# Kernel optimization log

Measured on AMD Instinct MI355X. Metric: run time of the kernel, lower is better.

## Reference

```python
import jax, jax.numpy as jnp
import numpy as np

NUM_LAYERS = 3

def setup_inputs() -> dict:
    key = jax.random.key(0)
    ku, ki, ke1, ke2 = jax.random.split(key, 4)
    num_users, num_items, D, E = 100000, 50000, 128, 1000000
    # xavier-uniform-ish init scale for the embedding tables
    bound = float(np.sqrt(6.0 / (num_users + D)))
    user_w = jax.random.uniform(ku, (num_users, D), jnp.float32, -bound, bound)
    bound_i = float(np.sqrt(6.0 / (num_items + D)))
    item_w = jax.random.uniform(ki, (num_items, D), jnp.float32, -bound_i, bound_i)
    # bipartite edges: user -> item (item ids offset by num_users), plus reverse direction
    u = jax.random.randint(ke1, (E,), 0, num_users, dtype=jnp.int32)
    v = jax.random.randint(ke2, (E,), 0, num_items, dtype=jnp.int32) + num_users
    edge_index = jnp.stack([jnp.concatenate([u, v]), jnp.concatenate([v, u])])  # [2, 2E]
    return {"user_w": user_w, "item_w": item_w, "edge_index": edge_index,
            "num_users": num_users, "num_items": num_items}

def reference(user_w, item_w, edge_index, num_users, num_items):
    n_nodes = num_users + num_items
    src, dst = edge_index[0], edge_index[1]
    # degree via scatter-add (duplicate edges sum, same as coalesce)
    deg = jax.ops.segment_sum(jnp.ones_like(src, dtype=user_w.dtype), src,
                              num_segments=n_nodes)
    dinv = jnp.where(deg > 0, deg ** -0.5, 0.0)
    dinv = jnp.where(jnp.isfinite(dinv), dinv, 0.0)
    vals = dinv[src] * dinv[dst]  # normalized adjacency values, [2E]

    emb = jnp.concatenate([user_w, item_w], axis=0)  # [n_nodes, D]
    acc = emb
    x = emb
    for _ in range(NUM_LAYERS):
        # SpMM: out[s] += vals(e) * x[dst(e)]
        x = jax.ops.segment_sum(vals[:, None] * x[dst], src, num_segments=n_nodes)
        acc = acc + x
    final = acc / jnp.asarray(NUM_LAYERS + 1, dtype=emb.dtype)
    return final[:num_users], final[num_users:]
```

## Files before the change

### kernel.cpp

```cpp
#include <hip/hip_runtime.h>
#include <hip/hip_fp16.h>
#include <cstdint>
#include <cstddef>

#define D 128
#define BSH 9
#define BNODES 512
#define NBMAX 512
#define CCHUNK 8192


__global__ __launch_bounds__(256)
void k_hist(const int* __restrict__ src, int* __restrict__ bhist, int ne2, int nb) {
    __shared__ int lc[NBMAX];
    for (int i = threadIdx.x; i < nb; i += 256) lc[i] = 0;
    __syncthreads();
    int base = blockIdx.x * CCHUNK;
    int lim = min(base + CCHUNK, ne2);
    for (int e = base + threadIdx.x; e < lim; e += 256)
        atomicAdd(&lc[src[e] >> BSH], 1);
    __syncthreads();
    for (int i = threadIdx.x; i < nb; i += 256)
        if (lc[i]) atomicAdd(&bhist[i], lc[i]);
}

__global__ void k_bscan(const int* __restrict__ bhist, int* __restrict__ bbase,
                        int* __restrict__ bfill, int* __restrict__ rp,
                        int nb, int nn, int ne2) {
    __shared__ int a[NBMAX], b2[NBMAX];
    int t = threadIdx.x;
    int v = (t < nb) ? bhist[t] : 0;
    a[t] = v;
    __syncthreads();
    int* cur = a; int* nxt = b2;
    for (int o = 1; o < NBMAX; o <<= 1) {
        int x = cur[t];
        if (t >= o) x += cur[t - o];
        nxt[t] = x;
        __syncthreads();
        int* tm = cur; cur = nxt; nxt = tm;
    }
    int excl = cur[t] - v;
    if (t < nb) { bbase[t] = excl; bfill[t] = excl; }
    if (t == 0) { bbase[nb] = ne2; rp[nn] = ne2; }
}

__global__ __launch_bounds__(256)
void k_scatter(const int* __restrict__ src, const int* __restrict__ dst,
               int* __restrict__ bfill, int2* __restrict__ tmp, int ne2, int nb) {
    __shared__ int lc[NBMAX], lb[NBMAX];
    for (int i = threadIdx.x; i < nb; i += 256) lc[i] = 0;
    __syncthreads();
    int base = blockIdx.x * CCHUNK;
    int rec[CCHUNK / 256];
#pragma unroll
    for (int i = 0; i < CCHUNK / 256; ++i) {
        int e = base + i * 256 + threadIdx.x;
        rec[i] = -1;
        if (e < ne2) {
            int b = src[e] >> BSH;
            int r = atomicAdd(&lc[b], 1);
            rec[i] = (r << BSH) | b;
        }
    }
    __syncthreads();
    for (int i = threadIdx.x; i < nb; i += 256)
        if (lc[i]) lb[i] = atomicAdd(&bfill[i], lc[i]);
    __syncthreads();
#pragma unroll
    for (int i = 0; i < CCHUNK / 256; ++i) {
        if (rec[i] >= 0) {
            int e = base + i * 256 + threadIdx.x;
            int b = rec[i] & (BNODES - 1);
            int r = rec[i] >> BSH;
            tmp[lb[b] + r] = make_int2(src[e], dst[e]);
        }
    }
}

__global__ __launch_bounds__(256)
void k_build(const int2* __restrict__ tmp, const int* __restrict__ bbase,
             int* __restrict__ col, int* __restrict__ rp, float* __restrict__ dinv,
             int nn) {
    __shared__ int cnt[BNODES];
    __shared__ int off[BNODES];
    __shared__ int wtot[4], woff[4];
    int bkt = blockIdx.x;
    int n0 = bkt << BSH;
    int nloc = min(BNODES, nn - n0);
    int ebeg = bbase[bkt], eend = bbase[bkt + 1];
    for (int i = threadIdx.x; i < BNODES; i += 256) cnt[i] = 0;
    __syncthreads();
    for (int e = ebeg + threadIdx.x; e < eend; e += 256)
        atomicAdd(&cnt[tmp[e].x - n0], 1);
    __syncthreads();
    int t = threadIdx.x;
    int c0 = cnt[2 * t], c1 = cnt[2 * t + 1];
    int s = c0 + c1;
    int lane = t & 63, wid = t >> 6;
    int x = s;
#pragma unroll
    for (int o = 1; o < 64; o <<= 1) {
        int y = __shfl_up(x, o);
        if (lane >= o) x += y;
    }
    if (lane == 63) wtot[wid] = x;
    __syncthreads();
    if (t == 0) { int a = 0; for (int k = 0; k < 4; ++k) { woff[k] = a; a += wtot[k]; } }
    __syncthreads();
    int eb = woff[wid] + x - s;
    off[2 * t] = eb;
    off[2 * t + 1] = eb + c0;
    __syncthreads();
    for (int i = threadIdx.x; i < nloc; i += 256) {
        rp[n0 + i] = ebeg + off[i];
        int c = cnt[i];
        dinv[n0 + i] = (c > 0) ? rsqrtf((float)c) : 0.0f;
    }
    __syncthreads();
    for (int i = threadIdx.x; i < BNODES; i += 256) cnt[i] = 0;
    __syncthreads();
    for (int e = ebeg + threadIdx.x; e < eend; e += 256) {
        int2 ed = tmp[e];
        int sl = ed.x - n0;
        int r = atomicAdd(&cnt[sl], 1);
        col[ebeg + off[sl] + r] = ed.y;
    }
}


__global__ void k_tohalf(const float2* __restrict__ uw, const float2* __restrict__ iw,
                         __half2* __restrict__ x0, int nu2, int ntot2) {
    int g = blockIdx.x * blockDim.x + threadIdx.x;
    if (g < ntot2) {
        float2 v = (g < nu2) ? uw[g] : iw[g - nu2];
        x0[g] = __floats2half2_rn(v.x, v.y);
    }
}

template <bool FUSE>
__global__ __launch_bounds__(256)
void k_spmm(const float4* __restrict__ xin, float4* __restrict__ xout,
            const int* __restrict__ rp, const int* __restrict__ col,
            const float* __restrict__ dinv,
            const float4* __restrict__ uw, const float4* __restrict__ iw,
            const float4* __restrict__ x1h, float4* __restrict__ outp,
            int nu, int nn) {
    int wave = (blockIdx.x * blockDim.x + threadIdx.x) >> 6;
    int lane = threadIdx.x & 63;
    int g = lane >> 4, l16 = lane & 15;
    int node = wave * 4 + g;
    int beg = 0, end = 0;
    if (node < nn) { beg = rp[node]; end = rp[node + 1]; }
    float acc[8];
#pragma unroll
    for (int k = 0; k < 8; ++k) acc[k] = 0.f;

    int srcl = g << 4;
    for (int base = beg; base < end; base += 16) {
        int p = base + l16;
        int d = 0;
        float wt = 0.f;
        if (p < end) {
            d = col[p];
            wt = dinv[d];
        }
        int m = min(16, end - base);
#pragma unroll 8
        for (int t = 0; t < m; ++t) {
            int dd = __shfl(d, srcl + t);
            float wv = __shfl(wt, srcl + t);
            float4 rv = xin[(size_t)dd * 16 + l16];
            const __half2* hp = reinterpret_cast<const __half2*>(&rv);
#pragma unroll
            for (int k = 0; k < 4; ++k) {
                float2 f = __half22float2(hp[k]);
                acc[2 * k]     = fmaf(wv, f.x, acc[2 * k]);
                acc[2 * k + 1] = fmaf(wv, f.y, acc[2 * k + 1]);
            }
        }
    }
    if (node >= nn) return;
    float s = dinv[node];
    if (!FUSE) {
        __half2 h[4];
#pragma unroll
        for (int k = 0; k < 4; ++k)
            h[k] = __floats2half2_rn(s * acc[2 * k], s * acc[2 * k + 1]);
        xout[(size_t)node * 16 + l16] = *reinterpret_cast<const float4*>(h);
    } else {
        size_t r16 = (size_t)node * 16 + l16;
        float4 av = x1h[r16];
        float4 bv = xin[r16];
        const __half2* ap = reinterpret_cast<const __half2*>(&av);
        const __half2* bp = reinterpret_cast<const __half2*>(&bv);
        float4 e0, e1;
        if (node < nu) {
            size_t rr = (size_t)node * 32 + 2 * l16;
            e0 = uw[rr]; e1 = uw[rr + 1];
        } else {
            size_t rr = (size_t)(node - nu) * 32 + 2 * l16;
            e0 = iw[rr]; e1 = iw[rr + 1];
        }
        float o[8];
#pragma unroll
        for (int k = 0; k < 4; ++k) {
            float2 fa = __half22float2(ap[k]);
            float2 fb = __half22float2(bp[k]);
            o[2 * k]     = fa.x + fb.x + s * acc[2 * k];
            o[2 * k + 1] = fa.y + fb.y + s * acc[2 * k + 1];
        }
        float4 w0 = make_float4(0.25f * (e0.x + o[0]), 0.25f * (e0.y + o[1]),
                                0.25f * (e0.z + o[2]), 0.25f * (e0.w + o[3]));
        float4 w1 = make_float4(0.25f * (e1.x + o[4]), 0.25f * (e1.y + o[5]),
                                0.25f * (e1.z + o[6]), 0.25f * (e1.w + o[7]));
        size_t r32 = (size_t)node * 32 + 2 * l16;
        outp[r32] = w0;
        outp[r32 + 1] = w1;
    }
}


extern "C" void kernel_launch(void* const* d_in, const int* in_sizes, int n_in,
                              void* d_out, int out_size, void* d_ws, size_t ws_size,
                              hipStream_t stream) {
    const float* uw = (const float*)d_in[0];
    const float* iw = (const float*)d_in[1];
    const int* ei = (const int*)d_in[2];

    const int NU = in_sizes[0] / D;
    const int NI = in_sizes[1] / D;
    const int NN = NU + NI;
    const int NE2 = in_sizes[2] / 2;
    const int* src = ei;
    const int* dst = ei + NE2;
    const int NB = (NN + BNODES - 1) >> BSH;

    char* p = (char*)d_ws;
    auto alloc = [&](size_t bytes) -> void* {
        void* r = (void*)p;
        p += (bytes + 255) & ~(size_t)255;
        return r;
    };
    int* bhist  = (int*)alloc(NBMAX * 4);
    int* bbase  = (int*)alloc((NBMAX + 1) * 4);
    int* bfill  = (int*)alloc(NBMAX * 4);
    int* rp     = (int*)alloc((size_t)(NN + 1) * 4);
    float* dinv = (float*)alloc((size_t)NN * 4);
    int2* tmp   = (int2*)alloc((size_t)NE2 * 8);
    int* col    = (int*)alloc((size_t)NE2 * 4);
    __half2* xa = (__half2*)alloc((size_t)NN * D * 2);
    __half2* xb = (__half2*)alloc((size_t)NN * D * 2);
    __half2* xc = (__half2*)alloc((size_t)NN * D * 2);
    float* outp = (float*)d_out;

    hipMemsetAsync(bhist, 0, NBMAX * 4, stream);

    int bce = (NE2 + CCHUNK - 1) / CCHUNK;
    k_hist<<<bce, 256, 0, stream>>>(src, bhist, NE2, NB);
    k_bscan<<<1, NBMAX, 0, stream>>>(bhist, bbase, bfill, rp, NB, NN, NE2);
    k_scatter<<<bce, 256, 0, stream>>>(src, dst, bfill, tmp, NE2, NB);
    k_build<<<NB, 256, 0, stream>>>(tmp, bbase, col, rp, dinv, NN);

    int ntot2 = NN * (D / 2);
    int nu2 = NU * (D / 2);
    int bi = (ntot2 + 255) / 256;
    k_tohalf<<<bi, 256, 0, stream>>>((const float2*)uw, (const float2*)iw, xa, nu2, ntot2);

    int bs = (NN + 15) / 16;
    k_spmm<false><<<bs, 256, 0, stream>>>((const float4*)xa, (float4*)xb, rp, col, dinv,
                                          nullptr, nullptr, nullptr, nullptr, NU, NN);
    k_spmm<false><<<bs, 256, 0, stream>>>((const float4*)xb, (float4*)xc, rp, col, dinv,
                                          nullptr, nullptr, nullptr, nullptr, NU, NN);
    k_spmm<true><<<bs, 256, 0, stream>>>((const float4*)xc, nullptr, rp, col, dinv,
                                         (const float4*)uw, (const float4*)iw,
                                         (const float4*)xb, (float4*)outp, NU, NN);
}
```

Measured before the change: 462.2 us.

## Rescale SpMM layers to drop per-edge dinv gather; fuse histogram with fp16 conversion

Layers two and three now work in a rescaled space (y = x / dinv). The inner loop becomes a plain sum with no per-edge dinv[d] gather or weight shuffle, and each row is scaled once by 1/deg. The final layer rebuilds the true values by multiplying with sqrt(deg) and reads the fp16 x0 in place of the fp32 embeddings. The histogram and fp16-conversion kernels are merged into one launch, and two extra per-node arrays are built; storing rescaled values in fp16 may shift rounding error.

Result: faster. 442.5 us (-4.3%).

```diff
diff --git a/kernel.cpp b/kernel.cpp
--- a/kernel.cpp
+++ b/kernel.cpp
@@ -11,17 +11,28 @@
 
 
 __global__ __launch_bounds__(256)
-void k_hist(const int* __restrict__ src, int* __restrict__ bhist, int ne2, int nb) {
-    __shared__ int lc[NBMAX];
-    for (int i = threadIdx.x; i < nb; i += 256) lc[i] = 0;
-    __syncthreads();
-    int base = blockIdx.x * CCHUNK;
-    int lim = min(base + CCHUNK, ne2);
-    for (int e = base + threadIdx.x; e < lim; e += 256)
-        atomicAdd(&lc[src[e] >> BSH], 1);
-    __syncthreads();
-    for (int i = threadIdx.x; i < nb; i += 256)
-        if (lc[i]) atomicAdd(&bhist[i], lc[i]);
+void k_hist_tohalf(const int* __restrict__ src, int* __restrict__ bhist,
+                   int ne2, int nb, int nbh,
+                   const float2* __restrict__ uw, const float2* __restrict__ iw,
+                   __half2* __restrict__ x0, int nu2, int ntot2) {
+    if ((int)blockIdx.x < nbh) {
+        __shared__ int lc[NBMAX];
+        for (int i = threadIdx.x; i < nb; i += 256) lc[i] = 0;
+        __syncthreads();
+        int base = blockIdx.x * CCHUNK;
+        int lim = min(base + CCHUNK, ne2);
+        for (int e = base + threadIdx.x; e < lim; e += 256)
+            atomicAdd(&lc[src[e] >> BSH], 1);
+        __syncthreads();
+        for (int i = threadIdx.x; i < nb; i += 256)
+            if (lc[i]) atomicAdd(&bhist[i], lc[i]);
+    } else {
+        int g = (blockIdx.x - nbh) * 256 + threadIdx.x;
+        if (g < ntot2) {
+            float2 v = (g < nu2) ? uw[g] : iw[g - nu2];
+            x0[g] = __floats2half2_rn(v.x, v.y);
+        }
+    }
 }
 
 __global__ void k_bscan(const int* __restrict__ bhist, int* __restrict__ bbase,
@@ -81,7 +92,7 @@
 __global__ __launch_bounds__(256)
 void k_build(const int2* __restrict__ tmp, const int* __restrict__ bbase,
              int* __restrict__ col, int* __restrict__ rp, float* __restrict__ dinv,
-             int nn) {
+             float* __restrict__ dinv2, float* __restrict__ rinv, int nn) {
     __shared__ int cnt[BNODES];
     __shared__ int off[BNODES];
     __shared__ int wtot[4], woff[4];
@@ -115,7 +126,10 @@
     for (int i = threadIdx.x; i < nloc; i += 256) {
         rp[n0 + i] = ebeg + off[i];
         int c = cnt[i];
-        dinv[n0 + i] = (c > 0) ? rsqrtf((float)c) : 0.0f;
+        float fc = (float)c;
+        dinv[n0 + i]  = (c > 0) ? rsqrtf(fc) : 0.0f;
+        dinv2[n0 + i] = (c > 0) ? 1.0f / fc : 0.0f;
+        rinv[n0 + i]  = (c > 0) ? sqrtf(fc) : 0.0f;
     }
     __syncthreads();
     for (int i = threadIdx.x; i < BNODES; i += 256) cnt[i] = 0;
@@ -128,24 +142,14 @@
     }
 }
 
-
-__global__ void k_tohalf(const float2* __restrict__ uw, const float2* __restrict__ iw,
-                         __half2* __restrict__ x0, int nu2, int ntot2) {
-    int g = blockIdx.x * blockDim.x + threadIdx.x;
-    if (g < ntot2) {
-        float2 v = (g < nu2) ? uw[g] : iw[g - nu2];
-        x0[g] = __floats2half2_rn(v.x, v.y);
-    }
-}
-
-template <bool FUSE>
+template <int MODE>
 __global__ __launch_bounds__(256)
 void k_spmm(const float4* __restrict__ xin, float4* __restrict__ xout,
             const int* __restrict__ rp, const int* __restrict__ col,
-            const float* __restrict__ dinv,
-            const float4* __restrict__ uw, const float4* __restrict__ iw,
-            const float4* __restrict__ x1h, float4* __restrict__ outp,
-            int nu, int nn) {
+            const float* __restrict__ dinv, const float* __restrict__ dinv2,
+            const float* __restrict__ rinv,
+            const float4* __restrict__ x0h, const float4* __restrict__ y1h,
+            float4* __restrict__ outp, int nn) {
     int wave = (blockIdx.x * blockDim.x + threadIdx.x) >> 6;
     int lane = threadIdx.x & 63;
     int g = lane >> 4, l16 = lane & 15;
@@ -163,57 +167,60 @@
         float wt = 0.f;
         if (p < end) {
             d = col[p];
-            wt = dinv[d];
+            if (MODE == 0) wt = dinv[d];
         }
         int m = min(16, end - base);
 #pragma unroll 8
         for (int t = 0; t < m; ++t) {
             int dd = __shfl(d, srcl + t);
-            float wv = __shfl(wt, srcl + t);
             float4 rv = xin[(size_t)dd * 16 + l16];
             const __half2* hp = reinterpret_cast<const __half2*>(&rv);
-#pragma unroll
-            for (int k = 0; k < 4; ++k) {
-                float2 f = __half22float2(hp[k]);
-                acc[2 * k]     = fmaf(wv, f.x, acc[2 * k]);
-                acc[2 * k + 1] = fmaf(wv, f.y, acc[2 * k + 1]);
+            if (MODE == 0) {
+                float wv = __shfl(wt, srcl + t);
+#pragma unroll
+                for (int k = 0; k < 4; ++k) {
+                    float2 f = __half22float2(hp[k]);
+                    acc[2 * k]     = fmaf(wv, f.x, acc[2 * k]);
+                    acc[2 * k + 1] = fmaf(wv, f.y, acc[2 * k + 1]);
+                }
+            } else {
+#pragma unroll
+                for (int k = 0; k < 4; ++k) {
+                    float2 f = __half22float2(hp[k]);
+                    acc[2 * k]     += f.x;
+                    acc[2 * k + 1] += f.y;
+                }
             }
         }
     }
     if (node >= nn) return;
-    float s = dinv[node];
-    if (!FUSE) {
+    float s2 = dinv2[node];
+    if (MODE != 2) {
         __half2 h[4];
 #pragma unroll
         for (int k = 0; k < 4; ++k)
-            h[k] = __floats2half2_rn(s * acc[2 * k], s * acc[2 * k + 1]);
+            h[k] = __floats2half2_rn(s2 * acc[2 * k], s2 * acc[2 * k + 1]);
         xout[(size_t)node * 16 + l16] = *reinterpret_cast<const float4*>(h);
     } else {
         size_t r16 = (size_t)node * 16 + l16;
-        float4 av = x1h[r16];
+        float4 ev = x0h[r16];
+        float4 av = y1h[r16];
         float4 bv = xin[r16];
+        const __half2* ep = reinterpret_cast<const __half2*>(&ev);
         const __half2* ap = reinterpret_cast<const __half2*>(&av);
         const __half2* bp = reinterpret_cast<const __half2*>(&bv);
-        float4 e0, e1;
-        if (node < nu) {
-            size_t rr = (size_t)node * 32 + 2 * l16;
-            e0 = uw[rr]; e1 = uw[rr + 1];
-        } else {
-            size_t rr = (size_t)(node - nu) * 32 + 2 * l16;
-            e0 = iw[rr]; e1 = iw[rr + 1];
-        }
+        float rv = rinv[node];
         float o[8];
 #pragma unroll
         for (int k = 0; k < 4; ++k) {
+            float2 fe = __half22float2(ep[k]);
             float2 fa = __half22float2(ap[k]);
             float2 fb = __half22float2(bp[k]);
-            o[2 * k]     = fa.x + fb.x + s * acc[2 * k];
-            o[2 * k + 1] = fa.y + fb.y + s * acc[2 * k + 1];
-        }
-        float4 w0 = make_float4(0.25f * (e0.x + o[0]), 0.25f * (e0.y + o[1]),
-                                0.25f * (e0.z + o[2]), 0.25f * (e0.w + o[3]));
-        float4 w1 = make_float4(0.25f * (e1.x + o[4]), 0.25f * (e1.y + o[5]),
-                                0.25f * (e1.z + o[6]), 0.25f * (e1.w + o[7]));
+            o[2 * k]     = 0.25f * (fe.x + (fa.x + fb.x + s2 * acc[2 * k]) * rv);
+            o[2 * k + 1] = 0.25f * (fe.y + (fa.y + fb.y + s2 * acc[2 * k + 1]) * rv);
+        }
+        float4 w0 = make_float4(o[0], o[1], o[2], o[3]);
+        float4 w1 = make_float4(o[4], o[5], o[6], o[7]);
         size_t r32 = (size_t)node * 32 + 2 * l16;
         outp[r32] = w0;
         outp[r32 + 1] = w1;
@@ -247,6 +254,8 @@
     int* bfill  = (int*)alloc(NBMAX * 4);
     int* rp     = (int*)alloc((size_t)(NN + 1) * 4);
     float* dinv = (float*)alloc((size_t)NN * 4);
+    float* dinv2= (float*)alloc((size_t)NN * 4);
+    float* rinv = (float*)alloc((size_t)NN * 4);
     int2* tmp   = (int2*)alloc((size_t)NE2 * 8);
     int* col    = (int*)alloc((size_t)NE2 * 4);
     __half2* xa = (__half2*)alloc((size_t)NN * D * 2);
@@ -256,23 +265,25 @@
 
     hipMemsetAsync(bhist, 0, NBMAX * 4, stream);
 
+    int ntot2 = NN * (D / 2);
+    int nu2 = NU * (D / 2);
     int bce = (NE2 + CCHUNK - 1) / CCHUNK;
-    k_hist<<<bce, 256, 0, stream>>>(src, bhist, NE2, NB);
+    int bi = (ntot2 + 255) / 256;
+
+    k_hist_tohalf<<<bce + bi, 256, 0, stream>>>(src, bhist, NE2, NB, bce,
+                                                (const float2*)uw, (const float2*)iw,
+                                                xa, nu2, ntot2);
     k_bscan<<<1, NBMAX, 0, stream>>>(bhist, bbase, bfill, rp, NB, NN, NE2);
     k_scatter<<<bce, 256, 0, stream>>>(src, dst, bfill, tmp, NE2, NB);
-    k_build<<<NB, 256, 0, stream>>>(tmp, bbase, col, rp, dinv, NN);
-
-    int ntot2 = NN * (D / 2);
-    int nu2 = NU * (D / 2);
-    int bi = (ntot2 + 255) / 256;
-    k_tohalf<<<bi, 256, 0, stream>>>((const float2*)uw, (const float2*)iw, xa, nu2, ntot2);
+    k_build<<<NB, 256, 0, stream>>>(tmp, bbase, col, rp, dinv, dinv2, rinv, NN);
 
     int bs = (NN + 15) / 16;
-    k_spmm<false><<<bs, 256, 0, stream>>>((const float4*)xa, (float4*)xb, rp, col, dinv,
-                                          nullptr, nullptr, nullptr, nullptr, NU, NN);
-    k_spmm<false><<<bs, 256, 0, stream>>>((const float4*)xb, (float4*)xc, rp, col, dinv,
-                                          nullptr, nullptr, nullptr, nullptr, NU, NN);
-    k_spmm<true><<<bs, 256, 0, stream>>>((const float4*)xc, nullptr, rp, col, dinv,
-                                         (const float4*)uw, (const float4*)iw,
-                                         (const float4*)xb, (float4*)outp, NU, NN);
-}
+    k_spmm<0><<<bs, 256, 0, stream>>>((const float4*)xa, (float4*)xb, rp, col,
+                                      dinv, dinv2, rinv, nullptr, nullptr, nullptr, NN);
+    k_spmm<1><<<bs, 256, 0, stream>>>((const float4*)xb, (float4*)xc, rp, col,
+                                      dinv, dinv2, rinv, nullptr, nullptr, nullptr, NN);
+    k_spmm<2><<<bs, 256, 0, stream>>>((const float4*)xc, nullptr, rp, col,
+                                      dinv, dinv2, rinv,
+                                      (const float4*)xa, (const float4*)xb,
+                                      (float4*)outp, NN);
+}
```
